# Performance work log

Hardware: AMD Instinct MI355X
Metric: run time of the kernel (lower is better)

## Reference

```python
import jax, jax.numpy as jnp
import numpy as np

N = 100000
E = 3200000
F_IN, H1, H2, C = 512, 32, 16, 11


def setup_inputs() -> dict:
    key = jax.random.key(0)
    ks = jax.random.split(key, 8)
    x = jax.random.normal(ks[0], (N, F_IN), dtype=jnp.float32)
    edge_index = jax.random.randint(ks[1], (2, E), 0, N, dtype=jnp.int64)
    def glorot(k, fan_in, fan_out):
        lim = np.sqrt(6.0 / (fan_in + fan_out)).astype(np.float32)
        return jax.random.uniform(k, (fan_in, fan_out), jnp.float32, -lim, lim)
    return {
        "x": x,
        "edge_index": edge_index,
        "W1": glorot(ks[2], F_IN, H1), "b1": jnp.zeros((H1,), jnp.float32),
        "W2": glorot(ks[3], H1, H2),   "b2": jnp.zeros((H2,), jnp.float32),
        "W3": glorot(ks[4], H2, C),    "b3": jnp.zeros((C,), jnp.float32),
    }


def _gcn_conv(x, W, b, src, dst, deg_inv_sqrt):
    # GCNConv: D^{-1/2}(A+I)D^{-1/2} X W + b, self-loops handled analytically.
    h = x @ W                                   # [N, out]
    norm = deg_inv_sqrt[src] * deg_inv_sqrt[dst]  # [E]
    msg = h[src] * norm[:, None]                # gather + scale
    agg = jax.ops.segment_sum(msg, dst, num_segments=x.shape[0])
    agg = agg + h * (deg_inv_sqrt ** 2)[:, None]  # self-loop term
    return agg + b


def reference(x, edge_index, W1, b1, W2, b2, W3, b3):
    src, dst = edge_index[0], edge_index[1]
    n = x.shape[0]
    # degree with self-loops, counted on destination (PyG convention)
    deg = jax.ops.segment_sum(jnp.ones((dst.shape[0],), x.dtype), dst, num_segments=n) + 1.0
    deg_inv_sqrt = jax.lax.rsqrt(deg)
    h = jax.nn.relu(_gcn_conv(x, W1, b1, src, dst, deg_inv_sqrt))
    # F.dropout(training=self.training) is identity in eval mode
    h = jax.nn.relu(_gcn_conv(h, W2, b2, src, dst, deg_inv_sqrt))
    h = _gcn_conv(h, W3, b3, src, dst, deg_inv_sqrt)
    return jax.nn.log_softmax(h, axis=1)
```

## Files before the change

### kernel.cpp

```cpp
#include <hip/hip_runtime.h>
#include <hip/hip_bf16.h>

static __device__ __forceinline__ unsigned short f2bf(float f) {
    unsigned u = __float_as_uint(f);
    unsigned r = (u + 0x7FFF + ((u >> 16) & 1)) >> 16;
    return (unsigned short)r;
}
static __device__ __forceinline__ float bflo(unsigned v) { return __uint_as_float(v << 16); }
static __device__ __forceinline__ float bfhi(unsigned v) { return __uint_as_float(v & 0xFFFF0000u); }
static __device__ __forceinline__ unsigned pack2bf(float a, float b) {
    __hip_bfloat162 h2 = __float22bfloat162_rn(float2{a, b});
    union { __hip_bfloat162 h; unsigned u; } cv;
    cv.h = h2;
    return cv.u;
}

typedef __attribute__((ext_vector_type(8))) short bf16x8;
typedef __attribute__((ext_vector_type(8))) unsigned short u16x8;
typedef __attribute__((ext_vector_type(4))) float f32x4;

#define BKT_SHIFT 7
#define BKT_NODES 128
#define CHUNK 16384

__global__ __launch_bounds__(512) void hist_wconv(const int* __restrict__ dst, int* __restrict__ histG,
                                                  const float* __restrict__ W, unsigned short* __restrict__ W1T,
                                                  int B, int NB, int E) {
    if ((int)blockIdx.x >= B) {
        int gidx = (blockIdx.x - B) * 512 + threadIdx.x;
        if (gidx < 32 * 512) {
            int c = gidx >> 9, k = gidx & 511;
            W1T[gidx] = f2bf(W[(size_t)k * 32 + c]);
        }
        return;
    }
    __shared__ int hist[1024];
    int tid = threadIdx.x;
    for (int i = tid; i < NB; i += 512) hist[i] = 0;
    __syncthreads();
    int base = blockIdx.x * CHUNK;
    for (int i = tid; i < CHUNK; i += 512) {
        int e = base + i;
        if (e >= E) break;
        atomicAdd(&hist[dst[e] >> BKT_SHIFT], 1);
    }
    __syncthreads();
    for (int i = tid; i < NB; i += 512) histG[(size_t)i * B + blockIdx.x] = hist[i];
}

__global__ __launch_bounds__(512) void scatter_k(const int* __restrict__ src, const int* __restrict__ dst,
                                                 const int* __restrict__ scanG, const int* __restrict__ blksum,
                                                 int* __restrict__ pairs, int B, int NB, int E) {
    __shared__ int sbase[1024];
    __shared__ int scnt[1024];
    int tid = threadIdx.x;
    for (int i = tid; i < NB; i += 512) {
        size_t idx = (size_t)i * B + blockIdx.x;
        sbase[i] = scanG[idx] + blksum[idx >> 11];
        scnt[i] = 0;
    }
    __syncthreads();
    int base = blockIdx.x * CHUNK;
    for (int i = tid; i < CHUNK; i += 512) {
        int e = base + i;
        if (e >= E) break;
        int d = dst[e], s = src[e];
        int b = d >> BKT_SHIFT;
        int r = atomicAdd(&scnt[b], 1);
        pairs[sbase[b] + r] = (s << BKT_SHIFT) | (d & (BKT_NODES - 1));
    }
}

#define SCAN_VPT 8
#define SCAN_ELEMS 2048

__global__ __launch_bounds__(256) void scan1(const int* __restrict__ in, int* __restrict__ out,
                                             int* __restrict__ blksum, int n) {
    __shared__ int sh[256];
    int base = blockIdx.x * SCAN_ELEMS + threadIdx.x * SCAN_VPT;
    int v[SCAN_VPT];
    int sum = 0;
    #pragma unroll
    for (int j = 0; j < SCAN_VPT; ++j) {
        v[j] = (base + j < n) ? in[base + j] : 0;
        sum += v[j];
    }
    sh[threadIdx.x] = sum;
    __syncthreads();
    for (int off = 1; off < 256; off <<= 1) {
        int t = (threadIdx.x >= off) ? sh[threadIdx.x - off] : 0;
        __syncthreads();
        sh[threadIdx.x] += t;
        __syncthreads();
    }
    if (threadIdx.x == 255) blksum[blockIdx.x] = sh[255];
    int run = sh[threadIdx.x] - sum;
    #pragma unroll
    for (int j = 0; j < SCAN_VPT; ++j) {
        if (base + j < n) out[base + j] = run;
        run += v[j];
    }
}

__global__ __launch_bounds__(256) void scan2(int* __restrict__ blksum, int nb) {
    __shared__ int sh[256];
    int t = threadIdx.x;
    int v = (t < nb) ? blksum[t] : 0;
    sh[t] = v;
    __syncthreads();
    for (int off = 1; off < 256; off <<= 1) {
        int u = (t >= off) ? sh[t - off] : 0;
        __syncthreads();
        sh[t] += u;
        __syncthreads();
    }
    if (t < nb) blksum[t] = sh[t] - v;
}

#define SORT_CAP 8192

__global__ __launch_bounds__(512) void sort_bucket(const int* __restrict__ pairs,
        const int* __restrict__ scanG, const int* __restrict__ blksum, int B, int NB,
        int* __restrict__ csr_src, int* __restrict__ node_start,
        int* __restrict__ cnt, float* __restrict__ dis, int n, int E) {
    __shared__ int keys[SORT_CAP];
    __shared__ int lcnt[BKT_NODES];
    __shared__ int lscan[BKT_NODES];
    __shared__ int lfill[BKT_NODES];
    int bkt = blockIdx.x, tid = threadIdx.x;
    size_t idx0 = (size_t)bkt * B;
    int e0 = scanG[idx0] + blksum[idx0 >> 11];
    int e1 = E;
    if (bkt + 1 < NB) {
        size_t idx1 = (size_t)(bkt + 1) * B;
        e1 = scanG[idx1] + blksum[idx1 >> 11];
    }
    int m = e1 - e0;
    if (tid < BKT_NODES) { lcnt[tid] = 0; lfill[tid] = 0; }
    __syncthreads();
    for (int i = tid; i < m; i += 512) {
        int k = pairs[e0 + i];
        if (i < SORT_CAP) keys[i] = k;
        atomicAdd(&lcnt[k & (BKT_NODES - 1)], 1);
    }
    __syncthreads();
    if (tid < 64) {
        int c0 = lcnt[2 * tid], c1 = lcnt[2 * tid + 1];
        int s = c0 + c1;
        #pragma unroll
        for (int off = 1; off < 64; off <<= 1) {
            int t = __shfl_up(s, off);
            if (tid >= off) s += t;
        }
        lscan[2 * tid]     = s - c1 - c0;
        lscan[2 * tid + 1] = s - c1;
    }
    __syncthreads();
    int nb0 = bkt << BKT_SHIFT;
    if (tid < BKT_NODES && nb0 + tid < n) {
        int deg = lcnt[tid];
        node_start[nb0 + tid] = e0 + lscan[tid];
        cnt[nb0 + tid] = deg;
        dis[nb0 + tid] = rsqrtf((float)deg + 1.0f);
    }
    for (int i = tid; i < m; i += 512) {
        int k = (i < SORT_CAP) ? keys[i] : pairs[e0 + i];
        int d = k & (BKT_NODES - 1);
        int pos = lscan[d] + atomicAdd(&lfill[d], 1);
        csr_src[e0 + pos] = k >> BKT_SHIFT;
    }
}


__global__ __launch_bounds__(512) void gemm1_mfma(const float* __restrict__ x, const unsigned short* __restrict__ W1T,
                                                  const float* __restrict__ dis, unsigned short* __restrict__ g, int n) {
    __shared__ __attribute__((aligned(16))) unsigned short wT[32][520];
    __shared__ __attribute__((aligned(16))) unsigned short xb[128][72];
    int tid = threadIdx.x;
    int node0 = blockIdx.x * 128;

    #pragma unroll
    for (int r = 0; r < 4; ++r) {
        int u8 = tid + r * 512;
        int c = u8 >> 6, kq = (u8 & 63) * 8;
        *(u16x8*)(&wT[c][kq]) = *(const u16x8*)(W1T + (size_t)c * 512 + kq);
    }

    int wv_ = tid >> 6;
    int lane = tid & 63;
    int mrow = lane & 15;
    int kg = lane >> 4;
    f32x4 acc0 = {0.f, 0.f, 0.f, 0.f};
    f32x4 acc1 = {0.f, 0.f, 0.f, 0.f};

    for (int k0 = 0; k0 < 512; k0 += 64) {
        __syncthreads();
        #pragma unroll
        for (int r = 0; r < 4; ++r) {
            int fi = tid + r * 512;
            int nd = fi >> 4, kq = (fi & 15) * 4;
            int gn = min(node0 + nd, n - 1);
            float4 xv = *(const float4*)(x + (size_t)gn * 512 + k0 + kq);
            uint2 pw;
            pw.x = pack2bf(xv.x, xv.y);
            pw.y = pack2bf(xv.z, xv.w);
            *(uint2*)(&xb[nd][kq]) = pw;
        }
        __syncthreads();
        #pragma unroll
        for (int ks = 0; ks < 2; ++ks) {
            bf16x8 a  = *(const bf16x8*)(&xb[wv_ * 16 + mrow][ks * 32 + kg * 8]);
            bf16x8 b0 = *(const bf16x8*)(&wT[mrow][k0 + ks * 32 + kg * 8]);
            bf16x8 b1 = *(const bf16x8*)(&wT[16 + mrow][k0 + ks * 32 + kg * 8]);
            acc0 = __builtin_amdgcn_mfma_f32_16x16x32_bf16(a, b0, acc0, 0, 0, 0);
            acc1 = __builtin_amdgcn_mfma_f32_16x16x32_bf16(a, b1, acc1, 0, 0, 0);
        }
    }
    #pragma unroll
    for (int j = 0; j < 4; ++j) {
        int node = node0 + wv_ * 16 + kg * 4 + j;
        if (node < n) {
            float dv = dis[node];
            g[(size_t)node * 32 + mrow]      = f2bf(acc0[j] * dv);
            g[(size_t)node * 32 + 16 + mrow] = f2bf(acc1[j] * dv);
        }
    }
}


__global__ __launch_bounds__(256) void gather1(const int* __restrict__ csr_src,
        const int* __restrict__ start, const int* __restrict__ cnt,
        const unsigned short* __restrict__ g1, const float* __restrict__ dis,
        const float* __restrict__ b1, const float* __restrict__ W2,
        unsigned short* __restrict__ g2, int n) {
    __shared__ float w2t[16 * 33];
    for (int i = threadIdx.x; i < 512; i += 256) {
        int k = i >> 4, c = i & 15;
        w2t[c * 33 + k] = W2[i];
    }
    __syncthreads();
    int node = blockIdx.x * 4 + (threadIdx.x >> 6);
    if (node >= n) return;
    int lane = threadIdx.x & 63;
    int fq = lane & 7;
    int j = lane >> 3;
    int i0 = start[node], i1 = i0 + cnt[node];
    float a0 = 0.f, a1 = 0.f, a2 = 0.f, a3 = 0.f;
    int i = i0 + j;
    for (; i + 24 < i1; i += 32) {
        int s1 = csr_src[i];
        int s2 = csr_src[i + 8];
        int s3 = csr_src[i + 16];
        int s4 = csr_src[i + 24];
        uint2 v1 = *(const uint2*)(g1 + (size_t)s1 * 32 + fq * 4);
        uint2 v2 = *(const uint2*)(g1 + (size_t)s2 * 32 + fq * 4);
        uint2 v3 = *(const uint2*)(g1 + (size_t)s3 * 32 + fq * 4);
        uint2 v4 = *(const uint2*)(g1 + (size_t)s4 * 32 + fq * 4);
        a0 += bflo(v1.x) + bflo(v2.x) + bflo(v3.x) + bflo(v4.x);
        a1 += bfhi(v1.x) + bfhi(v2.x) + bfhi(v3.x) + bfhi(v4.x);
        a2 += bflo(v1.y) + bflo(v2.y) + bflo(v3.y) + bflo(v4.y);
        a3 += bfhi(v1.y) + bfhi(v2.y) + bfhi(v3.y) + bfhi(v4.y);
    }
    for (; i < i1; i += 8) {
        uint2 v = *(const uint2*)(g1 + (size_t)csr_src[i] * 32 + fq * 4);
        a0 += bflo(v.x); a1 += bfhi(v.x);
        a2 += bflo(v.y); a3 += bfhi(v.y);
    }
    #pragma unroll
    for (int m = 8; m < 64; m <<= 1) {
        a0 += __shfl_xor(a0, m); a1 += __shfl_xor(a1, m);
        a2 += __shfl_xor(a2, m); a3 += __shfl_xor(a3, m);
    }
    float dv = dis[node];
    uint2 sv = *(const uint2*)(g1 + (size_t)node * 32 + fq * 4);
    float v0 = fmaxf((a0 + bflo(sv.x)) * dv + b1[4 * fq + 0], 0.f);
    float v1f = fmaxf((a1 + bfhi(sv.x)) * dv + b1[4 * fq + 1], 0.f);
    float v2f = fmaxf((a2 + bflo(sv.y)) * dv + b1[4 * fq + 2], 0.f);
    float v3f = fmaxf((a3 + bfhi(sv.y)) * dv + b1[4 * fq + 3], 0.f);
    int c = lane & 15;
    int j3 = lane >> 4;
    float p = 0.f;
    #pragma unroll
    for (int kk = 0; kk < 8; ++kk) {
        int k = j3 * 8 + kk;
        int srcl = k >> 2;
        float xk;
        if ((kk & 3) == 0) xk = __shfl(v0, srcl);
        else if ((kk & 3) == 1) xk = __shfl(v1f, srcl);
        else if ((kk & 3) == 2) xk = __shfl(v2f, srcl);
        else xk = __shfl(v3f, srcl);
        p = fmaf(xk, w2t[c * 33 + k], p);
    }
    p += __shfl_xor(p, 16);
    p += __shfl_xor(p, 32);
    if (lane < 16) g2[(size_t)node * 16 + c] = f2bf(p * dv);
}


__global__ __launch_bounds__(256) void gather2(const int* __restrict__ csr_src,
        const int* __restrict__ start, const int* __restrict__ cnt,
        const unsigned short* __restrict__ g2, const float* __restrict__ dis,
        const float* __restrict__ b2, const float* __restrict__ W3,
        unsigned short* __restrict__ g3, int n) {
    __shared__ float w3t[16 * 17];
    if (threadIdx.x < 256) {
        int k = threadIdx.x >> 4, c = threadIdx.x & 15;
        w3t[c * 17 + k] = (c < 11) ? W3[(size_t)k * 11 + c] : 0.f;
    }
    __syncthreads();
    int node = blockIdx.x * 4 + (threadIdx.x >> 6);
    if (node >= n) return;
    int lane = threadIdx.x & 63;
    int fq = lane & 3;
    int j = lane >> 2;
    int i0 = start[node], i1 = i0 + cnt[node];
    float a0 = 0.f, a1 = 0.f, a2 = 0.f, a3 = 0.f;
    int i = i0 + j;
    for (; i + 16 < i1; i += 32) {
        int s1 = csr_src[i];
        int s2 = csr_src[i + 16];
        uint2 v1 = *(const uint2*)(g2 + (size_t)s1 * 16 + fq * 4);
        uint2 v2 = *(const uint2*)(g2 + (size_t)s2 * 16 + fq * 4);
        a0 += bflo(v1.x) + bflo(v2.x);
        a1 += bfhi(v1.x) + bfhi(v2.x);
        a2 += bflo(v1.y) + bflo(v2.y);
        a3 += bfhi(v1.y) + bfhi(v2.y);
    }
    if (i < i1) {
        uint2 v = *(const uint2*)(g2 + (size_t)csr_src[i] * 16 + fq * 4);
        a0 += bflo(v.x); a1 += bfhi(v.x);
        a2 += bflo(v.y); a3 += bfhi(v.y);
    }
    #pragma unroll
    for (int m = 4; m < 64; m <<= 1) {
        a0 += __shfl_xor(a0, m); a1 += __shfl_xor(a1, m);
        a2 += __shfl_xor(a2, m); a3 += __shfl_xor(a3, m);
    }
    float dv = dis[node];
    uint2 sv = *(const uint2*)(g2 + (size_t)node * 16 + fq * 4);
    float v0 = fmaxf((a0 + bflo(sv.x)) * dv + b2[4 * fq + 0], 0.f);
    float v1f = fmaxf((a1 + bfhi(sv.x)) * dv + b2[4 * fq + 1], 0.f);
    float v2f = fmaxf((a2 + bflo(sv.y)) * dv + b2[4 * fq + 2], 0.f);
    float v3f = fmaxf((a3 + bfhi(sv.y)) * dv + b2[4 * fq + 3], 0.f);
    int c = lane & 15;
    int j2 = lane >> 4;
    float p = 0.f;
    {
        float xk0 = __shfl(v0, j2);
        float xk1 = __shfl(v1f, j2);
        float xk2 = __shfl(v2f, j2);
        float xk3 = __shfl(v3f, j2);
        p = fmaf(xk0, w3t[c * 17 + j2 * 4 + 0], p);
        p = fmaf(xk1, w3t[c * 17 + j2 * 4 + 1], p);
        p = fmaf(xk2, w3t[c * 17 + j2 * 4 + 2], p);
        p = fmaf(xk3, w3t[c * 17 + j2 * 4 + 3], p);
    }
    p += __shfl_xor(p, 16);
    p += __shfl_xor(p, 32);
    if (lane < 16) g3[(size_t)node * 16 + c] = f2bf(p * dv);
}


__global__ __launch_bounds__(256) void gather3(const int* __restrict__ csr_src,
        const int* __restrict__ start, const int* __restrict__ cnt,
        const unsigned short* __restrict__ g, const float* __restrict__ dis,
        const float* __restrict__ bias, float* __restrict__ out, int n) {
    int node = blockIdx.x * 4 + (threadIdx.x >> 6);
    if (node >= n) return;
    int lane = threadIdx.x & 63;
    int fq = lane & 3;
    int j = lane >> 2;
    int i0 = start[node], i1 = i0 + cnt[node];
    float a0 = 0.f, a1 = 0.f, a2 = 0.f, a3 = 0.f;
    int i = i0 + j;
    for (; i + 16 < i1; i += 32) {
        int s1 = csr_src[i];
        int s2 = csr_src[i + 16];
        uint2 v1 = *(const uint2*)(g + (size_t)s1 * 16 + fq * 4);
        uint2 v2 = *(const uint2*)(g + (size_t)s2 * 16 + fq * 4);
        a0 += bflo(v1.x) + bflo(v2.x);
        a1 += bfhi(v1.x) + bfhi(v2.x);
        a2 += bflo(v1.y) + bflo(v2.y);
        a3 += bfhi(v1.y) + bfhi(v2.y);
    }
    if (i < i1) {
        uint2 v = *(const uint2*)(g + (size_t)csr_src[i] * 16 + fq * 4);
        a0 += bflo(v.x); a1 += bfhi(v.x);
        a2 += bflo(v.y); a3 += bfhi(v.y);
    }
    #pragma unroll
    for (int m = 4; m < 64; m <<= 1) {
        a0 += __shfl_xor(a0, m); a1 += __shfl_xor(a1, m);
        a2 += __shfl_xor(a2, m); a3 += __shfl_xor(a3, m);
    }
    float dvn = dis[node];
    uint2 sv = *(const uint2*)(g + (size_t)node * 16 + fq * 4);
    int f0 = 4 * fq;
    bool ok0 = f0 + 0 < 11, ok1 = f0 + 1 < 11, ok2 = f0 + 2 < 11, ok3 = f0 + 3 < 11;
    float v0 = (a0 + bflo(sv.x)) * dvn + (ok0 ? bias[f0 + 0] : 0.f);
    float v1f = (a1 + bfhi(sv.x)) * dvn + (ok1 ? bias[f0 + 1] : 0.f);
    float v2f = (a2 + bflo(sv.y)) * dvn + (ok2 ? bias[f0 + 2] : 0.f);
    float v3f = (a3 + bfhi(sv.y)) * dvn + (ok3 ? bias[f0 + 3] : 0.f);
    const float NEG = -3.0e38f;
    float m0 = fmaxf(fmaxf(ok0 ? v0 : NEG, ok1 ? v1f : NEG),
                     fmaxf(ok2 ? v2f : NEG, ok3 ? v3f : NEG));
    m0 = fmaxf(m0, __shfl_xor(m0, 1));
    m0 = fmaxf(m0, __shfl_xor(m0, 2));
    float s = (ok0 ? __expf(v0 - m0) : 0.f) + (ok1 ? __expf(v1f - m0) : 0.f)
            + (ok2 ? __expf(v2f - m0) : 0.f) + (ok3 ? __expf(v3f - m0) : 0.f);
    s += __shfl_xor(s, 1);
    s += __shfl_xor(s, 2);
    float ls = __logf(s) + m0;
    if (lane < 4) {
        float* orow = out + (size_t)node * 11 + f0;
        if (ok0) orow[0] = v0 - ls;
        if (ok1) orow[1] = v1f - ls;
        if (ok2) orow[2] = v2f - ls;
        if (ok3) orow[3] = v3f - ls;
    }
}


extern "C" void kernel_launch(void* const* d_in, const int* in_sizes, int n_in,
                              void* d_out, int out_size, void* d_ws, size_t ws_size,
                              hipStream_t stream) {
    const float* x  = (const float*)d_in[0];
    const int*   ei = (const int*)d_in[1];
    const float* W1 = (const float*)d_in[2];
    const float* b1 = (const float*)d_in[3];
    const float* W2 = (const float*)d_in[4];
    const float* b2 = (const float*)d_in[5];
    const float* W3 = (const float*)d_in[6];
    const float* b3 = (const float*)d_in[7];
    float* out = (float*)d_out;

    const int n = in_sizes[0] / 512;
    const int E = in_sizes[1] / 2;
    const int* src = ei;
    const int* dst = ei + E;

    const int NB = (n + BKT_NODES - 1) >> BKT_SHIFT;
    const int B  = (E + CHUNK - 1) / CHUNK;
    const int NBB = NB * B;
    const int nb_scan = (NBB + SCAN_ELEMS - 1) / SCAN_ELEMS;

    int* ws0 = (int*)d_ws;
    size_t off = 0;
    int*   cnt     = ws0 + off; off += (size_t)n;
    float* dis     = (float*)(ws0 + off); off += (size_t)n;
    int*   nstart  = ws0 + off; off += (size_t)n;
    int*   scanG   = ws0 + off; off += (size_t)NBB;
    int*   blksum  = ws0 + off; off += 256;
    int*   pairs   = ws0 + off; off += (size_t)E;
    int*   csr_src = ws0 + off; off += (size_t)E;
    unsigned short* g1 = (unsigned short*)(ws0 + off); off += (size_t)n * 16;
    unsigned short* g2 = (unsigned short*)(ws0 + off); off += (size_t)n * 8;
    unsigned short* g3 = (unsigned short*)(ws0 + off); off += (size_t)n * 8;
    unsigned short* W1T = (unsigned short*)(ws0 + off); off += 8192;
    int*   histG   = (int*)g1;

    hist_wconv<<<B + 32, 512, 0, stream>>>(dst, histG, W1, W1T, B, NB, E);
    scan1<<<nb_scan, 256, 0, stream>>>(histG, scanG, blksum, NBB);
    scan2<<<1, 256, 0, stream>>>(blksum, nb_scan);
    scatter_k<<<B, 512, 0, stream>>>(src, dst, scanG, blksum, pairs, B, NB, E);
    sort_bucket<<<NB, 512, 0, stream>>>(pairs, scanG, blksum, B, NB, csr_src, nstart, cnt, dis, n, E);

    gemm1_mfma<<<(n + 127) / 128, 512, 0, stream>>>(x, W1T, dis, g1, n);
    gather1<<<(n + 3) / 4, 256, 0, stream>>>(csr_src, nstart, cnt, g1, dis, b1, W2, g2, n);
    gather2<<<(n + 3) / 4, 256, 0, stream>>>(csr_src, nstart, cnt, g2, dis, b2, W3, g3, n);
    gather3<<<(n + 3) / 4, 256, 0, stream>>>(csr_src, nstart, cnt, g3, dis, b3, out, n);
}
```

Measured before the change: 283.1 us.

## Fold block-sum scan into consumers, pack node start/count, prefetch GEMM tiles

Removes the single-block scan2 launch by having scatter_k and sort_bucket each compute the exclusive prefix of blksum in one wavefront via shuffles. Node start and degree are packed into one int2 array so each gather kernel does a single 8-byte load per node instead of two loads. The gemm1 x-tile load is register double-buffered so the next k-slice global load overlaps the MFMA work. The trade-off is redundant prefix work in every block and extra registers in the GEMM; the in-block prefix only covers up to 128 scan blocks.

```diff
diff --git a/kernel.cpp b/kernel.cpp
--- a/kernel.cpp
+++ b/kernel.cpp
@@ -50,13 +50,27 @@
 
 __global__ __launch_bounds__(512) void scatter_k(const int* __restrict__ src, const int* __restrict__ dst,
                                                  const int* __restrict__ scanG, const int* __restrict__ blksum,
-                                                 int* __restrict__ pairs, int B, int NB, int E) {
+                                                 int* __restrict__ pairs, int B, int NB, int E, int nbs) {
     __shared__ int sbase[1024];
     __shared__ int scnt[1024];
+    __shared__ int bpref[128];
     int tid = threadIdx.x;
+    if (tid < 64) {
+        int c0 = (2 * tid < nbs) ? blksum[2 * tid] : 0;
+        int c1 = (2 * tid + 1 < nbs) ? blksum[2 * tid + 1] : 0;
+        int s = c0 + c1;
+        #pragma unroll
+        for (int off = 1; off < 64; off <<= 1) {
+            int t = __shfl_up(s, off);
+            if (tid >= off) s += t;
+        }
+        bpref[2 * tid]     = s - c1 - c0;
+        bpref[2 * tid + 1] = s - c1;
+    }
+    __syncthreads();
     for (int i = tid; i < NB; i += 512) {
         size_t idx = (size_t)i * B + blockIdx.x;
-        sbase[i] = scanG[idx] + blksum[idx >> 11];
+        sbase[i] = scanG[idx] + bpref[idx >> 11];
         scnt[i] = 0;
     }
     __syncthreads();
@@ -102,42 +116,40 @@
     }
 }
 
-__global__ __launch_bounds__(256) void scan2(int* __restrict__ blksum, int nb) {
-    __shared__ int sh[256];
-    int t = threadIdx.x;
-    int v = (t < nb) ? blksum[t] : 0;
-    sh[t] = v;
-    __syncthreads();
-    for (int off = 1; off < 256; off <<= 1) {
-        int u = (t >= off) ? sh[t - off] : 0;
-        __syncthreads();
-        sh[t] += u;
-        __syncthreads();
-    }
-    if (t < nb) blksum[t] = sh[t] - v;
-}
-
 #define SORT_CAP 8192
 
 __global__ __launch_bounds__(512) void sort_bucket(const int* __restrict__ pairs,
         const int* __restrict__ scanG, const int* __restrict__ blksum, int B, int NB,
-        int* __restrict__ csr_src, int* __restrict__ node_start,
-        int* __restrict__ cnt, float* __restrict__ dis, int n, int E) {
+        int* __restrict__ csr_src, int2* __restrict__ nsc,
+        float* __restrict__ dis, int n, int E, int nbs) {
     __shared__ int keys[SORT_CAP];
     __shared__ int lcnt[BKT_NODES];
     __shared__ int lscan[BKT_NODES];
     __shared__ int lfill[BKT_NODES];
+    __shared__ int bpref[128];
     int bkt = blockIdx.x, tid = threadIdx.x;
+    if (tid < 64) {
+        int c0 = (2 * tid < nbs) ? blksum[2 * tid] : 0;
+        int c1 = (2 * tid + 1 < nbs) ? blksum[2 * tid + 1] : 0;
+        int s = c0 + c1;
+        #pragma unroll
+        for (int off = 1; off < 64; off <<= 1) {
+            int t = __shfl_up(s, off);
+            if (tid >= off) s += t;
+        }
+        bpref[2 * tid]     = s - c1 - c0;
+        bpref[2 * tid + 1] = s - c1;
+    }
+    if (tid < BKT_NODES) { lcnt[tid] = 0; lfill[tid] = 0; }
+    __syncthreads();
     size_t idx0 = (size_t)bkt * B;
-    int e0 = scanG[idx0] + blksum[idx0 >> 11];
+    int e0 = scanG[idx0] + bpref[idx0 >> 11];
     int e1 = E;
     if (bkt + 1 < NB) {
         size_t idx1 = (size_t)(bkt + 1) * B;
-        e1 = scanG[idx1] + blksum[idx1 >> 11];
+        e1 = scanG[idx1] + bpref[idx1 >> 11];
     }
     int m = e1 - e0;
-    if (tid < BKT_NODES) { lcnt[tid] = 0; lfill[tid] = 0; }
-    __syncthreads();
     for (int i = tid; i < m; i += 512) {
         int k = pairs[e0 + i];
         if (i < SORT_CAP) keys[i] = k;
@@ -159,8 +171,7 @@
     int nb0 = bkt << BKT_SHIFT;
     if (tid < BKT_NODES && nb0 + tid < n) {
         int deg = lcnt[tid];
-        node_start[nb0 + tid] = e0 + lscan[tid];
-        cnt[nb0 + tid] = deg;
+        nsc[nb0 + tid] = make_int2(e0 + lscan[tid], deg);
         dis[nb0 + tid] = rsqrtf((float)deg + 1.0f);
     }
     for (int i = tid; i < m; i += 512) {
@@ -193,20 +204,35 @@
     f32x4 acc0 = {0.f, 0.f, 0.f, 0.f};
     f32x4 acc1 = {0.f, 0.f, 0.f, 0.f};
 
+    int snd[4], skq[4];
+    const float* sptr[4];
+    #pragma unroll
+    for (int r = 0; r < 4; ++r) {
+        int fi = tid + r * 512;
+        snd[r] = fi >> 4;
+        skq[r] = (fi & 15) * 4;
+        int gn = min(node0 + snd[r], n - 1);
+        sptr[r] = x + (size_t)gn * 512 + skq[r];
+    }
+
+    float4 ra[4];
+    #pragma unroll
+    for (int r = 0; r < 4; ++r) ra[r] = *(const float4*)(sptr[r]);
+
     for (int k0 = 0; k0 < 512; k0 += 64) {
         __syncthreads();
         #pragma unroll
         for (int r = 0; r < 4; ++r) {
-            int fi = tid + r * 512;
-            int nd = fi >> 4, kq = (fi & 15) * 4;
-            int gn = min(node0 + nd, n - 1);
-            float4 xv = *(const float4*)(x + (size_t)gn * 512 + k0 + kq);
             uint2 pw;
-            pw.x = pack2bf(xv.x, xv.y);
-            pw.y = pack2bf(xv.z, xv.w);
-            *(uint2*)(&xb[nd][kq]) = pw;
+            pw.x = pack2bf(ra[r].x, ra[r].y);
+            pw.y = pack2bf(ra[r].z, ra[r].w);
+            *(uint2*)(&xb[snd[r]][skq[r]]) = pw;
         }
         __syncthreads();
+        if (k0 + 64 < 512) {
+            #pragma unroll
+            for (int r = 0; r < 4; ++r) ra[r] = *(const float4*)(sptr[r] + k0 + 64);
+        }
         #pragma unroll
         for (int ks = 0; ks < 2; ++ks) {
             bf16x8 a  = *(const bf16x8*)(&xb[wv_ * 16 + mrow][ks * 32 + kg * 8]);
@@ -229,7 +255,7 @@
 
 
 __global__ __launch_bounds__(256) void gather1(const int* __restrict__ csr_src,
-        const int* __restrict__ start, const int* __restrict__ cnt,
+        const int2* __restrict__ nsc,
         const unsigned short* __restrict__ g1, const float* __restrict__ dis,
         const float* __restrict__ b1, const float* __restrict__ W2,
         unsigned short* __restrict__ g2, int n) {
@@ -244,7 +270,8 @@
     int lane = threadIdx.x & 63;
     int fq = lane & 7;
     int j = lane >> 3;
-    int i0 = start[node], i1 = i0 + cnt[node];
+    int2 sc = nsc[node];
+    int i0 = sc.x, i1 = sc.x + sc.y;
     float a0 = 0.f, a1 = 0.f, a2 = 0.f, a3 = 0.f;
     int i = i0 + j;
     for (; i + 24 < i1; i += 32) {
@@ -298,7 +325,7 @@
 
 
 __global__ __launch_bounds__(256) void gather2(const int* __restrict__ csr_src,
-        const int* __restrict__ start, const int* __restrict__ cnt,
+        const int2* __restrict__ nsc,
         const unsigned short* __restrict__ g2, const float* __restrict__ dis,
         const float* __restrict__ b2, const float* __restrict__ W3,
         unsigned short* __restrict__ g3, int n) {
@@ -313,7 +340,8 @@
     int lane = threadIdx.x & 63;
     int fq = lane & 3;
     int j = lane >> 2;
-    int i0 = start[node], i1 = i0 + cnt[node];
+    int2 sc = nsc[node];
+    int i0 = sc.x, i1 = sc.x + sc.y;
     float a0 = 0.f, a1 = 0.f, a2 = 0.f, a3 = 0.f;
     int i = i0 + j;
     for (; i + 16 < i1; i += 32) {
@@ -362,7 +390,7 @@
 
 
 __global__ __launch_bounds__(256) void gather3(const int* __restrict__ csr_src,
-        const int* __restrict__ start, const int* __restrict__ cnt,
+        const int2* __restrict__ nsc,
         const unsigned short* __restrict__ g, const float* __restrict__ dis,
         const float* __restrict__ bias, float* __restrict__ out, int n) {
     int node = blockIdx.x * 4 + (threadIdx.x >> 6);
@@ -370,7 +398,8 @@
     int lane = threadIdx.x & 63;
     int fq = lane & 3;
     int j = lane >> 2;
-    int i0 = start[node], i1 = i0 + cnt[node];
+    int2 sc = nsc[node];
+    int i0 = sc.x, i1 = sc.x + sc.y;
     float a0 = 0.f, a1 = 0.f, a2 = 0.f, a3 = 0.f;
     int i = i0 + j;
     for (; i + 16 < i1; i += 32) {
@@ -446,9 +475,8 @@
 
     int* ws0 = (int*)d_ws;
     size_t off = 0;
-    int*   cnt     = ws0 + off; off += (size_t)n;
     float* dis     = (float*)(ws0 + off); off += (size_t)n;
-    int*   nstart  = ws0 + off; off += (size_t)n;
+    int2*  nsc     = (int2*)(ws0 + off);  off += (size_t)2 * n;
     int*   scanG   = ws0 + off; off += (size_t)NBB;
     int*   blksum  = ws0 + off; off += 256;
     int*   pairs   = ws0 + off; off += (size_t)E;
@@ -461,12 +489,11 @@
 
     hist_wconv<<<B + 32, 512, 0, stream>>>(dst, histG, W1, W1T, B, NB, E);
     scan1<<<nb_scan, 256, 0, stream>>>(histG, scanG, blksum, NBB);
-    scan2<<<1, 256, 0, stream>>>(blksum, nb_scan);
-    scatter_k<<<B, 512, 0, stream>>>(src, dst, scanG, blksum, pairs, B, NB, E);
-    sort_bucket<<<NB, 512, 0, stream>>>(pairs, scanG, blksum, B, NB, csr_src, nstart, cnt, dis, n, E);
+    scatter_k<<<B, 512, 0, stream>>>(src, dst, scanG, blksum, pairs, B, NB, E, nb_scan);
+    sort_bucket<<<NB, 512, 0, stream>>>(pairs, scanG, blksum, B, NB, csr_src, nsc, dis, n, E, nb_scan);
 
     gemm1_mfma<<<(n + 127) / 128, 512, 0, stream>>>(x, W1T, dis, g1, n);
-    gather1<<<(n + 3) / 4, 256, 0, stream>>>(csr_src, nstart, cnt, g1, dis, b1, W2, g2, n);
-    gather2<<<(n + 3) / 4, 256, 0, stream>>>(csr_src, nstart, cnt, g2, dis, b2, W3, g3, n);
-    gather3<<<(n + 3) / 4, 256, 0, stream>>>(csr_src, nstart, cnt, g3, dis, b3, out, n);
-}
+    gather1<<<(n + 3) / 4, 256, 0, stream>>>(csr_src, nsc, g1, dis, b1, W2, g2, n);
+    gather2<<<(n + 3) / 4, 256, 0, stream>>>(csr_src, nsc, g2, dis, b2, W3, g3, n);
+    gather3<<<(n + 3) / 4, 256, 0, stream>>>(csr_src, nsc, g3, dis, b3, out, n);
+}
```

Result: no change. 281.6 us (-0.5%).
